# Kernel optimization log

Hardware: AMD Instinct MI355X
Metric: run time of the kernel (lower is better)

The kernel has to match this reference:

```python
import jax, jax.numpy as jnp
import numpy as np

NUM_NODES = 50000
NUM_EDGES = 800000
NUM_GRAPHS = 500
D_IN = 128
D_HID = 128


def setup_inputs() -> dict:
    key = jax.random.key(0)
    ks = jax.random.split(key, 6)
    x = jax.random.normal(ks[0], (NUM_NODES, D_IN), dtype=jnp.float32)
    edge_index = jax.random.randint(ks[1], (2, NUM_EDGES), 0, NUM_NODES, dtype=jnp.int64)
    edge_weight = jax.random.uniform(ks[2], (NUM_EDGES,), dtype=jnp.float32)
    batch = jnp.sort(jax.random.randint(ks[3], (NUM_NODES,), 0, NUM_GRAPHS, dtype=jnp.int64))
    W = jax.random.normal(ks[4], (D_IN, D_HID), dtype=jnp.float32) * (1.0 / np.sqrt(D_IN))
    b = jnp.zeros((D_HID,), dtype=jnp.float32)
    return {"x": x, "edge_index": edge_index, "edge_weight": edge_weight, "batch": batch, "W": W, "b": b}


def reference(x, edge_index, edge_weight, batch, W, b):
    N = x.shape[0]
    # --- GCNConv (PyG semantics): add self-loops (weight 1), symmetric norm ---
    loops = jnp.arange(N, dtype=edge_index.dtype)
    row = jnp.concatenate([edge_index[0], loops])  # source j
    col = jnp.concatenate([edge_index[1], loops])  # target i
    w = jnp.concatenate([edge_weight, jnp.ones((N,), x.dtype)])
    deg = jax.ops.segment_sum(w, col, num_segments=N)            # weighted in-degree
    dinv = jnp.where(deg > 0, jax.lax.rsqrt(deg), 0.0)
    norm = dinv[row] * dinv[col] * w                             # [E+N]
    h = x @ W                                                    # [N, H] dense transform
    msg = h[row] * norm[:, None]                                 # gather + scale, [E+N, H]
    out = jax.ops.segment_sum(msg, col, num_segments=N) + b      # scatter-add, [N, H]
    # --- ReLU; dropout is identity at inference ---
    out = jax.nn.relu(out)
    # --- global mean pool over graphs in the batch ---
    sums = jax.ops.segment_sum(out, batch, num_segments=NUM_GRAPHS)
    cnt = jax.ops.segment_sum(jnp.ones((N,), out.dtype), batch, num_segments=NUM_GRAPHS)
    global_graph_emb = sums / jnp.maximum(cnt, 1.0)[:, None]     # [G, H]
    return out, global_graph_emb
```

## Files before the change

kernel.cpp:

```cpp
#include <hip/hip_runtime.h>
#include <hip/hip_fp16.h>


#define REPS 8

typedef _Float16 f16;
typedef _Float16 half8 __attribute__((ext_vector_type(8)));
typedef float f32x4 __attribute__((ext_vector_type(4)));

__global__ __launch_bounds__(256) void k_init(int* __restrict__ cnt4, int M4, int nzb,
                                              const float* __restrict__ W,
                                              f16* __restrict__ Wt) {
    int bid = blockIdx.x;
    int t = threadIdx.x;
    if (bid < nzb) {
        int i = bid * 256 + t;
        if (i < M4) ((int4*)cnt4)[i] = make_int4(0, 0, 0, 0);
    } else {
        int n = (bid - nzb) * 8 + (t >> 5);
        int k = (t & 31) * 4;
        union { f16 h[4]; uint2 u; } p;
#pragma unroll
        for (int j = 0; j < 4; ++j) p.h[j] = (f16)W[(k + j) * 128 + n];
        *(uint2*)&Wt[n * 128 + k] = p.u;
    }
}

__global__ __launch_bounds__(256) void k_count_pos(const int* __restrict__ ei,
                                                   int* cnt4, int* __restrict__ pos,
                                                   int E, int N) {
    int e = blockIdx.x * 256 + threadIdx.x;
    if (e < E) pos[e] = atomicAdd(&cnt4[(e & (REPS - 1)) * N + ei[E + e]], 1);
}

__global__ __launch_bounds__(256) void k_scan1(const int* __restrict__ cnt4,
                                               int* __restrict__ rp4,
                                               int* __restrict__ bsum, int M, int N) {
    __shared__ int wsum[4];
    int t = threadIdx.x;
    int k = blockIdx.x * 256 + t;
    int v = 0;
    if (k < M) v = cnt4[(k & (REPS - 1)) * N + (k / REPS)];
    int lane = t & 63, wid = t >> 6;
    int s = v;
#pragma unroll
    for (int o = 1; o < 64; o <<= 1) {
        int u = __shfl_up(s, o);
        if (lane >= o) s += u;
    }
    if (lane == 63) wsum[wid] = s;
    __syncthreads();
    int off = 0;
#pragma unroll
    for (int w = 0; w < 4; ++w)
        if (w < wid) off += wsum[w];
    if (k < M) rp4[k] = off + s - v;
    if (t == 255) bsum[blockIdx.x] = off + s;
}

__global__ __launch_bounds__(256) void k_scan3(int* __restrict__ rp4,
                                               const int* __restrict__ bsum,
                                               int M, int E) {
    __shared__ int wsum[4];
    int t = threadIdx.x;
    int bid = blockIdx.x;
    int s = 0;
    for (int j = t; j < bid; j += 256) s += bsum[j];
    int lane = t & 63, wid = t >> 6;
#pragma unroll
    for (int o = 1; o < 64; o <<= 1) s += __shfl_down(s, o);
    if (lane == 0) wsum[wid] = s;
    __syncthreads();
    int off = wsum[0] + wsum[1] + wsum[2] + wsum[3];
    int k = bid * 256 + t;
    if (k < M) rp4[k] += off;
    if (bid == 0 && t == 0) rp4[M] = E;
}

__global__ __launch_bounds__(256) void k_fill(const int* __restrict__ ei,
                                              const float* __restrict__ ew,
                                              const int* __restrict__ rp4,
                                              const int* __restrict__ pos,
                                              int2* __restrict__ srcval, int E) {
    int e = blockIdx.x * 256 + threadIdx.x;
    if (e >= E) return;
    int row = ei[e];
    int col = ei[E + e];
    int slot = rp4[col * REPS + (e & (REPS - 1))] + pos[e];
    srcval[slot] = make_int2(row, __float_as_int(ew[e]));
}

__global__ __launch_bounds__(256) void k_deg_csr(const int* __restrict__ rp4,
                                                 const int2* __restrict__ srcval,
                                                 float* __restrict__ dinv, int N) {
    __shared__ float sdeg[256];
    __shared__ int srp[257];
    int t = threadIdx.x;
    int n0 = blockIdx.x * 256;
    int nn = min(256, N - n0);
    if (nn <= 0) return;
    sdeg[t] = 1.0f;
    for (int i = t; i <= nn; i += 256) srp[i] = rp4[(n0 + i) * REPS];
    __syncthreads();
    int beg = srp[0], end = srp[nn];
    for (int j = beg + t; j < end; j += 256) {
        int2 sv = srcval[j];
        int lo = 0, hi = nn - 1;
        while (lo < hi) {
            int mid = (lo + hi + 1) >> 1;
            if (srp[mid] <= j) lo = mid; else hi = mid - 1;
        }
        atomicAdd(&sdeg[lo], __int_as_float(sv.y));
    }
    __syncthreads();
    if (t < nn) dinv[n0 + t] = rsqrtf(sdeg[t]);
}

__global__ __launch_bounds__(256) void k_gemm(const float* __restrict__ x,
                                              const f16* __restrict__ Wt,
                                              const float* __restrict__ dinv,
                                              f16* __restrict__ hh, int N) {
    __shared__ f16 sX[128 * 136];
    __shared__ f16 sW[128 * 136];
    int t = threadIdx.x;
    int row0 = blockIdx.x * 128;
#pragma unroll
    for (int it = 0; it < 8; ++it) {
        int i = t + 256 * it;
        int n = i >> 4, k8 = (i & 15) * 8;
        *(half8*)&sW[n * 136 + k8] = *(const half8*)&Wt[n * 128 + k8];
    }
#pragma unroll
    for (int it = 0; it < 16; ++it) {
        int i = t + 256 * it;
        int r = i >> 5, c4 = (i & 31) * 4;
        float4 xv = make_float4(0.f, 0.f, 0.f, 0.f);
        if (row0 + r < N) xv = *(const float4*)&x[(size_t)(row0 + r) * 128 + c4];
        union { f16 h[4]; uint2 u; } p;
        p.h[0] = (f16)xv.x; p.h[1] = (f16)xv.y; p.h[2] = (f16)xv.z; p.h[3] = (f16)xv.w;
        *(uint2*)&sX[r * 136 + c4] = p.u;
    }
    __syncthreads();

    int w = t >> 6, l = t & 63;
    int lm = l & 15, lg = l >> 4;
    f32x4 acc[2][8];
#pragma unroll
    for (int rt = 0; rt < 2; ++rt)
#pragma unroll
        for (int ct = 0; ct < 8; ++ct) acc[rt][ct] = (f32x4){0.f, 0.f, 0.f, 0.f};

    int arow = w * 32 + lm;
#pragma unroll
    for (int ks = 0; ks < 4; ++ks) {
        int ko = ks * 32 + lg * 8;
        half8 a0 = *(const half8*)&sX[arow * 136 + ko];
        half8 a1 = *(const half8*)&sX[(arow + 16) * 136 + ko];
#pragma unroll
        for (int ct = 0; ct < 8; ++ct) {
            half8 bf = *(const half8*)&sW[(ct * 16 + lm) * 136 + ko];
            acc[0][ct] = __builtin_amdgcn_mfma_f32_16x16x32_f16(a0, bf, acc[0][ct], 0, 0, 0);
            acc[1][ct] = __builtin_amdgcn_mfma_f32_16x16x32_f16(a1, bf, acc[1][ct], 0, 0, 0);
        }
    }

#pragma unroll
    for (int rt = 0; rt < 2; ++rt) {
#pragma unroll
        for (int r = 0; r < 4; ++r) {
            int lrow = w * 32 + rt * 16 + lg * 4 + r;
            int grow = row0 + lrow;
            float di = (grow < N) ? dinv[grow] : 0.f;
#pragma unroll
            for (int ct = 0; ct < 8; ++ct)
                sX[lrow * 136 + ct * 16 + lm] = (f16)(acc[rt][ct][r] * di);
        }
    }
#pragma unroll
    for (int it = 0; it < 8; ++it) {
        int i = l + 64 * it;
        int lr = i >> 4, k8 = (i & 15) * 8;
        int grow = row0 + w * 32 + lr;
        if (grow < N)
            *(half8*)&hh[(size_t)grow * 128 + k8] =
                *(const half8*)&sX[(w * 32 + lr) * 136 + k8];
    }
}

__global__ __launch_bounds__(256) void k_aggregate(const int2* __restrict__ srcval,
                                                   const int* __restrict__ rp4,
                                                   const f16* __restrict__ hh,
                                                   const float* __restrict__ dinv,
                                                   const float* __restrict__ b,
                                                   float* __restrict__ out, int N) {
    int node = blockIdx.x * 4 + (threadIdx.x >> 6);
    if (node >= N) return;
    int lane = threadIdx.x & 63;
    int g = lane >> 4;
    int lm = lane & 15;
    int d0 = lm * 8;
    int beg = rp4[node * REPS], end = rp4[(node + 1) * REPS];

    float acc0[8], acc1[8];
#pragma unroll
    for (int k = 0; k < 8; ++k) { acc0[k] = 0.f; acc1[k] = 0.f; }

    int j = beg;
    for (; j + 8 <= end; j += 8) {
        int2 ma = srcval[j + g];
        int2 mb = srcval[j + 4 + g];
        half8 va = *(const half8*)&hh[(size_t)ma.x * 128 + d0];
        half8 vb = *(const half8*)&hh[(size_t)mb.x * 128 + d0];
        float wa = __int_as_float(ma.y);
        float wb = __int_as_float(mb.y);
#pragma unroll
        for (int k = 0; k < 8; ++k) {
            acc0[k] = fmaf((float)va[k], wa, acc0[k]);
            acc1[k] = fmaf((float)vb[k], wb, acc1[k]);
        }
    }
    if (j + 4 <= end) {
        int2 ma = srcval[j + g];
        half8 va = *(const half8*)&hh[(size_t)ma.x * 128 + d0];
        float wa = __int_as_float(ma.y);
#pragma unroll
        for (int k = 0; k < 8; ++k) acc0[k] = fmaf((float)va[k], wa, acc0[k]);
        j += 4;
    }
    int r = end - j;
    if (r > 0) {
        int2 ma = srcval[j + min(g, r - 1)];
        float wa = (g < r) ? __int_as_float(ma.y) : 0.f;
        half8 va = *(const half8*)&hh[(size_t)ma.x * 128 + d0];
#pragma unroll
        for (int k = 0; k < 8; ++k) acc0[k] = fmaf((float)va[k], wa, acc0[k]);
    }

#pragma unroll
    for (int k = 0; k < 8; ++k) acc0[k] += acc1[k];
#pragma unroll
    for (int k = 0; k < 8; ++k) acc0[k] += __shfl_xor(acc0[k], 16);
#pragma unroll
    for (int k = 0; k < 8; ++k) acc0[k] += __shfl_xor(acc0[k], 32);

    if (g == 0) {
        float di = dinv[node];
        half8 hs = *(const half8*)&hh[(size_t)node * 128 + d0];
        float4 bv0 = *(const float4*)&b[d0];
        float4 bv1 = *(const float4*)&b[d0 + 4];
        float4 o0, o1;
        o0.x = fmaxf(fmaf(acc0[0] + (float)hs[0], di, bv0.x), 0.f);
        o0.y = fmaxf(fmaf(acc0[1] + (float)hs[1], di, bv0.y), 0.f);
        o0.z = fmaxf(fmaf(acc0[2] + (float)hs[2], di, bv0.z), 0.f);
        o0.w = fmaxf(fmaf(acc0[3] + (float)hs[3], di, bv0.w), 0.f);
        o1.x = fmaxf(fmaf(acc0[4] + (float)hs[4], di, bv1.x), 0.f);
        o1.y = fmaxf(fmaf(acc0[5] + (float)hs[5], di, bv1.y), 0.f);
        o1.z = fmaxf(fmaf(acc0[6] + (float)hs[6], di, bv1.z), 0.f);
        o1.w = fmaxf(fmaf(acc0[7] + (float)hs[7], di, bv1.w), 0.f);
        *(float4*)&out[(size_t)node * 128 + d0] = o0;
        *(float4*)&out[(size_t)node * 128 + d0 + 4] = o1;
    }
}

__global__ __launch_bounds__(256) void k_pool(const float* __restrict__ out,
                                              const int* __restrict__ batch,
                                              float* __restrict__ pool, int N, int G) {
    __shared__ float sacc[256];
    __shared__ int bounds[2];
    int g = blockIdx.x;
    int t = threadIdx.x;
    if (t < 2) {
        int target = g + t;
        int lo = 0, hi = N;
        while (lo < hi) {
            int mid = (lo + hi) >> 1;
            if (batch[mid] < target) lo = mid + 1; else hi = mid;
        }
        bounds[t] = lo;
    }
    __syncthreads();
    int lo = bounds[0], hi = bounds[1];
    int d = t & 127, r = t >> 7;
    float s = 0.f;
    for (int n = lo + r; n < hi; n += 2)
        s += out[(size_t)n * 128 + d];
    sacc[t] = s;
    __syncthreads();
    if (t < 128) {
        float tot = sacc[t] + sacc[t + 128];
        pool[(size_t)g * 128 + t] = tot / fmaxf((float)(hi - lo), 1.0f);
    }
}

extern "C" void kernel_launch(void* const* d_in, const int* in_sizes, int n_in,
                              void* d_out, int out_size, void* d_ws, size_t ws_size,
                              hipStream_t stream) {
    const float* x     = (const float*)d_in[0];
    const int*   ei    = (const int*)d_in[1];
    const float* ew    = (const float*)d_in[2];
    const int*   batch = (const int*)d_in[3];
    const float* W     = (const float*)d_in[4];
    const float* b     = (const float*)d_in[5];

    int N = in_sizes[3];
    int E = in_sizes[2];
    int G = (out_size - N * 128) / 128;
    int M = N * REPS;
    int nb1 = (M + 255) / 256;

    float* out  = (float*)d_out;
    float* pool = out + (size_t)N * 128;

    f16*    hh     = (f16*)d_ws;
    int2*   srcval = (int2*)(hh + (size_t)N * 128);
    float*  dinv   = (float*)(srcval + E);
    int*    cnt4   = (int*)(dinv + N);
    int*    rp4    = cnt4 + M;
    int*    bsum   = rp4 + M + 1;
    int*    pos    = bsum + nb1;
    f16*    Wt     = (f16*)(pos + E);

    int M4  = M / 4;
    int nzb = (M4 + 255) / 256;
    k_init<<<nzb + 16, 256, 0, stream>>>(cnt4, M4, nzb, W, Wt);
    k_count_pos<<<(E + 255) / 256, 256, 0, stream>>>(ei, cnt4, pos, E, N);
    k_scan1<<<nb1, 256, 0, stream>>>(cnt4, rp4, bsum, M, N);
    k_scan3<<<nb1, 256, 0, stream>>>(rp4, bsum, M, E);
    k_fill<<<(E + 255) / 256, 256, 0, stream>>>(ei, ew, rp4, pos, srcval, E);
    k_deg_csr<<<(N + 255) / 256, 256, 0, stream>>>(rp4, srcval, dinv, N);
    k_gemm<<<(N + 127) / 128, 256, 0, stream>>>(x, Wt, dinv, hh, N);
    k_aggregate<<<(N + 3) / 4, 256, 0, stream>>>(srcval, rp4, hh, dinv, b, out, N);
    k_pool<<<G, 256, 0, stream>>>(out, batch, pool, N, G);
}
```

Baseline: 150.8 us.

## Fold degree into count pass and replace block-offset add with single-block scan

```diff
diff --git a/kernel.cpp b/kernel.cpp
--- a/kernel.cpp
+++ b/kernel.cpp
@@ -8,14 +8,14 @@
 typedef _Float16 half8 __attribute__((ext_vector_type(8)));
 typedef float f32x4 __attribute__((ext_vector_type(4)));
 
-__global__ __launch_bounds__(256) void k_init(int* __restrict__ cnt4, int M4, int nzb,
+__global__ __launch_bounds__(256) void k_init(int* __restrict__ zbase, int Z4, int nzb,
                                               const float* __restrict__ W,
                                               f16* __restrict__ Wt) {
     int bid = blockIdx.x;
     int t = threadIdx.x;
     if (bid < nzb) {
         int i = bid * 256 + t;
-        if (i < M4) ((int4*)cnt4)[i] = make_int4(0, 0, 0, 0);
+        if (i < Z4) ((int4*)zbase)[i] = make_int4(0, 0, 0, 0);
     } else {
         int n = (bid - nzb) * 8 + (t >> 5);
         int k = (t & 31) * 4;
@@ -26,21 +26,27 @@
     }
 }
 
-__global__ __launch_bounds__(256) void k_count_pos(const int* __restrict__ ei,
-                                                   int* cnt4, int* __restrict__ pos,
-                                                   int E, int N) {
+__global__ __launch_bounds__(256) void k_count(const int* __restrict__ ei,
+                                               const float* __restrict__ ew,
+                                               int* cnt8, float* deg8f, int E, int N) {
     int e = blockIdx.x * 256 + threadIdx.x;
-    if (e < E) pos[e] = atomicAdd(&cnt4[(e & (REPS - 1)) * N + ei[E + e]], 1);
-}
-
-__global__ __launch_bounds__(256) void k_scan1(const int* __restrict__ cnt4,
+    if (e >= E) return;
+    int k = (e & (REPS - 1)) * N + ei[E + e];
+    atomicAdd(&cnt8[k], 1);
+    atomicAdd(&deg8f[k], ew[e]);
+}
+
+__global__ __launch_bounds__(256) void k_scan1(const int* __restrict__ cnt8,
+                                               const float* __restrict__ deg8f,
                                                int* __restrict__ rp4,
-                                               int* __restrict__ bsum, int M, int N) {
+                                               int* __restrict__ bsum,
+                                               float* __restrict__ dinv,
+                                               int M, int N) {
     __shared__ int wsum[4];
     int t = threadIdx.x;
     int k = blockIdx.x * 256 + t;
     int v = 0;
-    if (k < M) v = cnt4[(k & (REPS - 1)) * N + (k / REPS)];
+    if (k < M) v = cnt8[(k & (REPS - 1)) * N + (k >> 3)];
     int lane = t & 63, wid = t >> 6;
     int s = v;
 #pragma unroll
@@ -56,64 +62,61 @@
         if (w < wid) off += wsum[w];
     if (k < M) rp4[k] = off + s - v;
     if (t == 255) bsum[blockIdx.x] = off + s;
-}
-
-__global__ __launch_bounds__(256) void k_scan3(int* __restrict__ rp4,
-                                               const int* __restrict__ bsum,
-                                               int M, int E) {
+
+    int n = blockIdx.x * 256 + t;
+    if (n < N) {
+        float d = 1.0f;
+#pragma unroll
+        for (int r = 0; r < REPS; ++r) d += deg8f[r * N + n];
+        dinv[n] = rsqrtf(d);
+    }
+}
+
+__global__ __launch_bounds__(256) void k_scan2(int* __restrict__ bsum, int nb1) {
     __shared__ int wsum[4];
-    int t = threadIdx.x;
-    int bid = blockIdx.x;
-    int s = 0;
-    for (int j = t; j < bid; j += 256) s += bsum[j];
+    __shared__ int sCarry;
+    int t = threadIdx.x;
     int lane = t & 63, wid = t >> 6;
-#pragma unroll
-    for (int o = 1; o < 64; o <<= 1) s += __shfl_down(s, o);
-    if (lane == 0) wsum[wid] = s;
-    __syncthreads();
-    int off = wsum[0] + wsum[1] + wsum[2] + wsum[3];
-    int k = bid * 256 + t;
-    if (k < M) rp4[k] += off;
-    if (bid == 0 && t == 0) rp4[M] = E;
+    if (t == 0) sCarry = 0;
+    __syncthreads();
+    for (int base = 0; base < nb1; base += 256) {
+        int i = base + t;
+        int v = (i < nb1) ? bsum[i] : 0;
+        int s = v;
+#pragma unroll
+        for (int o = 1; o < 64; o <<= 1) {
+            int u = __shfl_up(s, o);
+            if (lane >= o) s += u;
+        }
+        if (lane == 63) wsum[wid] = s;
+        __syncthreads();
+        int off = 0;
+#pragma unroll
+        for (int w = 0; w < 4; ++w) if (w < wid) off += wsum[w];
+        int tot = wsum[0] + wsum[1] + wsum[2] + wsum[3];
+        int c = sCarry;
+        __syncthreads();
+        if (i < nb1) bsum[i] = c + off + s - v;
+        if (t == 0) sCarry = c + tot;
+        __syncthreads();
+    }
 }
 
 __global__ __launch_bounds__(256) void k_fill(const int* __restrict__ ei,
                                               const float* __restrict__ ew,
                                               const int* __restrict__ rp4,
-                                              const int* __restrict__ pos,
-                                              int2* __restrict__ srcval, int E) {
+                                              const int* __restrict__ bsum,
+                                              int* cnt8b,
+                                              int2* __restrict__ srcval, int E, int N) {
     int e = blockIdx.x * 256 + threadIdx.x;
     if (e >= E) return;
     int row = ei[e];
     int col = ei[E + e];
-    int slot = rp4[col * REPS + (e & (REPS - 1))] + pos[e];
+    int rep = e & (REPS - 1);
+    int k = col * REPS + rep;
+    int p = atomicAdd(&cnt8b[rep * N + col], 1);
+    int slot = rp4[k] + bsum[k >> 8] + p;
     srcval[slot] = make_int2(row, __float_as_int(ew[e]));
-}
-
-__global__ __launch_bounds__(256) void k_deg_csr(const int* __restrict__ rp4,
-                                                 const int2* __restrict__ srcval,
-                                                 float* __restrict__ dinv, int N) {
-    __shared__ float sdeg[256];
-    __shared__ int srp[257];
-    int t = threadIdx.x;
-    int n0 = blockIdx.x * 256;
-    int nn = min(256, N - n0);
-    if (nn <= 0) return;
-    sdeg[t] = 1.0f;
-    for (int i = t; i <= nn; i += 256) srp[i] = rp4[(n0 + i) * REPS];
-    __syncthreads();
-    int beg = srp[0], end = srp[nn];
-    for (int j = beg + t; j < end; j += 256) {
-        int2 sv = srcval[j];
-        int lo = 0, hi = nn - 1;
-        while (lo < hi) {
-            int mid = (lo + hi + 1) >> 1;
-            if (srp[mid] <= j) lo = mid; else hi = mid - 1;
-        }
-        atomicAdd(&sdeg[lo], __int_as_float(sv.y));
-    }
-    __syncthreads();
-    if (t < nn) dinv[n0 + t] = rsqrtf(sdeg[t]);
 }
 
 __global__ __launch_bounds__(256) void k_gemm(const float* __restrict__ x,
@@ -189,17 +192,21 @@
 
 __global__ __launch_bounds__(256) void k_aggregate(const int2* __restrict__ srcval,
                                                    const int* __restrict__ rp4,
+                                                   const int* __restrict__ bsum,
                                                    const f16* __restrict__ hh,
                                                    const float* __restrict__ dinv,
                                                    const float* __restrict__ b,
-                                                   float* __restrict__ out, int N) {
+                                                   float* __restrict__ out, int N, int M, int E) {
     int node = blockIdx.x * 4 + (threadIdx.x >> 6);
     if (node >= N) return;
     int lane = threadIdx.x & 63;
     int g = lane >> 4;
     int lm = lane & 15;
     int d0 = lm * 8;
-    int beg = rp4[node * REPS], end = rp4[(node + 1) * REPS];
+    int bk = node * REPS;
+    int ek = bk + REPS;
+    int beg = rp4[bk] + bsum[bk >> 8];
+    int end = (ek == M) ? E : rp4[ek] + bsum[ek >> 8];
 
     float acc0[8], acc1[8];
 #pragma unroll
@@ -314,21 +321,21 @@
     f16*    hh     = (f16*)d_ws;
     int2*   srcval = (int2*)(hh + (size_t)N * 128);
     float*  dinv   = (float*)(srcval + E);
-    int*    cnt4   = (int*)(dinv + N);
-    int*    rp4    = cnt4 + M;
-    int*    bsum   = rp4 + M + 1;
-    int*    pos    = bsum + nb1;
-    f16*    Wt     = (f16*)(pos + E);
-
-    int M4  = M / 4;
-    int nzb = (M4 + 255) / 256;
-    k_init<<<nzb + 16, 256, 0, stream>>>(cnt4, M4, nzb, W, Wt);
-    k_count_pos<<<(E + 255) / 256, 256, 0, stream>>>(ei, cnt4, pos, E, N);
-    k_scan1<<<nb1, 256, 0, stream>>>(cnt4, rp4, bsum, M, N);
-    k_scan3<<<nb1, 256, 0, stream>>>(rp4, bsum, M, E);
-    k_fill<<<(E + 255) / 256, 256, 0, stream>>>(ei, ew, rp4, pos, srcval, E);
-    k_deg_csr<<<(N + 255) / 256, 256, 0, stream>>>(rp4, srcval, dinv, N);
+    int*    cnt8   = (int*)(dinv + N);
+    int*    cnt8b  = cnt8 + M;
+    float*  deg8f  = (float*)(cnt8b + M);
+    int*    rp4    = (int*)(deg8f + M);
+    int*    bsum   = rp4 + M;
+    f16*    Wt     = (f16*)(((uintptr_t)(bsum + nb1) + 15) & ~(uintptr_t)15);
+
+    int Z4  = (3 * M) / 4;
+    int nzb = (Z4 + 255) / 256;
+    k_init<<<nzb + 16, 256, 0, stream>>>(cnt8, Z4, nzb, W, Wt);
+    k_count<<<(E + 255) / 256, 256, 0, stream>>>(ei, ew, cnt8, deg8f, E, N);
+    k_scan1<<<nb1, 256, 0, stream>>>(cnt8, deg8f, rp4, bsum, dinv, M, N);
+    k_scan2<<<1, 256, 0, stream>>>(bsum, nb1);
+    k_fill<<<(E + 255) / 256, 256, 0, stream>>>(ei, ew, rp4, bsum, cnt8b, srcval, E, N);
     k_gemm<<<(N + 127) / 128, 256, 0, stream>>>(x, Wt, dinv, hh, N);
-    k_aggregate<<<(N + 3) / 4, 256, 0, stream>>>(srcval, rp4, hh, dinv, b, out, N);
+    k_aggregate<<<(N + 3) / 4, 256, 0, stream>>>(srcval, rp4, bsum, hh, dinv, b, out, N, M, E);
     k_pool<<<G, 256, 0, stream>>>(out, batch, pool, N, G);
 }
```

Result: slower. 200.5 us (+32.9%).
